# Kernel optimization log

Measured on AMD Instinct MI355X. Metric: run time of the kernel, lower is better.

The kernel has to match this reference:

```python
import jax, jax.numpy as jnp
import numpy as np

N_HEAD = 16
T0 = 1.0        # eta schedule reference time
C_LOG = 3.0     # fixed eta(t) = C_LOG * log(t / T0)  (mode='log', non-learnable default)
ETA_CLIP = 50.0 # eta clamped to [-ETA_CLIP, ETA_CLIP] before exponentiation


def setup_inputs() -> dict:
    key = jax.random.key(0)
    k0, k1, k2 = jax.random.split(key, 3)
    B, T, D = 2, 2048, 1024
    x = jax.random.normal(k0, (B, T, D), dtype=jnp.float32)
    ln_weight = jnp.ones((D,), dtype=jnp.float32)  # LayerNorm weight (bias=False per cfg)
    c_attn_w = jax.random.normal(k1, (3 * D, D), dtype=jnp.float32) * 0.02  # torch Linear weight [3D, D]
    c_proj_w = jax.random.normal(k2, (D, D), dtype=jnp.float32) * 0.02      # output proj [D, D]
    # theta_h = inv_softplus(1.0) so that step size h = softplus(theta_h) = 1.0
    theta_h = jnp.asarray(np.log(np.expm1(1.0)), dtype=jnp.float32)
    return {"x": x, "ln_weight": ln_weight, "c_attn_w": c_attn_w,
            "c_proj_w": c_proj_w, "theta_h": theta_h}


def _layer_norm(x, w, eps=1e-5):
    mu = jnp.mean(x, axis=-1, keepdims=True)
    var = jnp.var(x, axis=-1, keepdims=True)
    return (x - mu) * jax.lax.rsqrt(var + eps) * w


def reference(x, ln_weight, c_attn_w, c_proj_w, theta_h):
    B, T, D = x.shape
    H = N_HEAD
    hd = D // H

    y = _layer_norm(x, ln_weight)
    qkv = jnp.einsum('btd,ed->bte', y, c_attn_w)        # [B, T, 3D]
    q, k, v = jnp.split(qkv, 3, axis=-1)
    q = q.reshape(B, T, H, hd).transpose(0, 2, 1, 3)    # [B, H, T, hd]
    k = k.reshape(B, T, H, hd).transpose(0, 2, 1, 3)
    v = v.reshape(B, T, H, hd).transpose(0, 2, 1, 3)

    # time-dependent conformal/symplectic scaling: t_i = t0 + h*i, eta = c_log*log(t/t0)
    h = jax.nn.softplus(theta_h)
    t = T0 + h * jnp.arange(T, dtype=jnp.float32)
    eta = jnp.clip(C_LOG * jnp.log(t / T0), -ETA_CLIP, ETA_CLIP)  # [T]
    q = q * jnp.exp(eta)[None, None, :, None]    # query scaled by exp(+eta(t_i))
    k = k * jnp.exp(-eta)[None, None, :, None]   # key scaled by exp(-eta(t_j))

    att = jnp.einsum('bhqd,bhkd->bhqk', q, k) / jnp.sqrt(jnp.float32(hd))
    mask = jnp.tril(jnp.ones((T, T), dtype=bool))  # causal: keep j <= i
    att = jnp.where(mask[None, None], att, -jnp.inf)
    att = jax.nn.softmax(att, axis=-1)

    out = jnp.einsum('bhqk,bhkd->bhqd', att, v)
    out = out.transpose(0, 2, 1, 3).reshape(B, T, D)
    return jnp.einsum('btd,ed->bte', out, c_proj_w)
```

## Files before the change

kernel.cpp:

```cpp
#include <hip/hip_runtime.h>
#include <stdint.h>
#include <stddef.h>

typedef __attribute__((ext_vector_type(8))) short short8;
typedef __attribute__((ext_vector_type(4))) float float4v;

#define T_SEQ 2048
#define D_MODEL 1024
#define NH 16
#define HD 64

static __device__ __forceinline__ unsigned short f2bf(float f) {
  unsigned u = __builtin_bit_cast(unsigned, f);
  u += 0x7fffu + ((u >> 16) & 1u);
  return (unsigned short)(u >> 16);
}
static __device__ __forceinline__ float bf2f(unsigned short h) {
  unsigned u = ((unsigned)h) << 16;
  return __builtin_bit_cast(float, u);
}
static __device__ __forceinline__ float4v mfma16(short8 a, short8 b, float4v c) {
  return __builtin_amdgcn_mfma_f32_16x16x32_bf16(a, b, c, 0, 0, 0);
}
static __device__ __forceinline__ void split3(float f, unsigned short& h0,
                                              unsigned short& h1, unsigned short& h2) {
  h0 = f2bf(f);
  float r1 = f - bf2f(h0);
  h1 = f2bf(r1);
  float r2 = r1 - bf2f(h1);
  h2 = f2bf(r2);
}
static __device__ __forceinline__ void split2(float f, unsigned short& h0, unsigned short& h1) {
  h0 = f2bf(f);
  h1 = f2bf(f - bf2f(h0));
}

static __device__ __forceinline__ void stage16(const unsigned short* g, unsigned short* l) {
#if __has_builtin(__builtin_amdgcn_global_load_lds)
  __builtin_amdgcn_global_load_lds(
      (const __attribute__((address_space(1))) unsigned int*)g,
      (__attribute__((address_space(3))) unsigned int*)l, 16, 0, 0);
#else
  *(short8*)l = *(const short8*)g;
#endif
}

__global__ void eta_kernel(const float* theta, float* E, float* Einv) {
  int i = blockIdx.x * blockDim.x + threadIdx.x;
  if (i >= T_SEQ) return;
  float th = theta[0];
  float h = log1pf(expf(th));
  float t = 1.0f + h * (float)i;
  float eta = 3.0f * logf(t);
  eta = fminf(fmaxf(eta, -50.0f), 50.0f);
  E[i] = expf(eta);
  Einv[i] = expf(-eta);
}

__global__ __launch_bounds__(256) void ln_kernel(const float* x, const float* wgt,
                          unsigned short* y0, unsigned short* y1, unsigned short* y2) {
  int row = blockIdx.x;
  int tid = threadIdx.x;
  const float* xr = x + (size_t)row * D_MODEL;
  float v[4];
  float sum = 0.f, ssq = 0.f;
  for (int it = 0; it < 4; ++it) {
    float f = xr[tid + 256 * it];
    v[it] = f;
    sum += f; ssq += f * f;
  }
  for (int off = 32; off >= 1; off >>= 1) {
    sum += __shfl_xor(sum, off, 64);
    ssq += __shfl_xor(ssq, off, 64);
  }
  __shared__ float rs[4], rq[4];
  int w = tid >> 6;
  if ((tid & 63) == 0) { rs[w] = sum; rq[w] = ssq; }
  __syncthreads();
  sum = rs[0] + rs[1] + rs[2] + rs[3];
  ssq = rq[0] + rq[1] + rq[2] + rq[3];
  float mu = sum * (1.0f / D_MODEL);
  float var = ssq * (1.0f / D_MODEL) - mu * mu;
  float rstd = rsqrtf(var + 1e-5f);
  for (int it = 0; it < 4; ++it) {
    int d = tid + 256 * it;
    float y = (v[it] - mu) * rstd * wgt[d];
    unsigned short h0, h1, h2;
    split3(y, h0, h1, h2);
    size_t o = (size_t)row * D_MODEL + d;
    y0[o] = h0; y1[o] = h1; y2[o] = h2;
  }
}

__global__ __launch_bounds__(256) void conv_w3(const float* src, unsigned short* W0,
                                               unsigned short* W1, unsigned short* W2) {
  size_t base = ((size_t)blockIdx.x * 256 + threadIdx.x) * 8;
  int row = (int)(base >> 10);
  short8 a, b, c;
  for (int j = 0; j < 8; ++j) {
    unsigned short h0, h1, h2;
    split3(src[base + j], h0, h1, h2);
    a[j] = (short)h0; b[j] = (short)h1; c[j] = (short)h2;
  }
  *(short8*)(W0 + base) = a;
  *(short8*)(W1 + base) = b;
  if (row < 2048) *(short8*)(W2 + base) = c;
}

__global__ __launch_bounds__(256) void conv_pw(const float* src, unsigned short* P0,
                                               unsigned short* P1) {
  size_t base = ((size_t)blockIdx.x * 256 + threadIdx.x) * 8;
  short8 a, b;
  for (int j = 0; j < 8; ++j) {
    unsigned short h0, h1;
    split2(src[base + j], h0, h1);
    a[j] = (short)h0; b[j] = (short)h1;
  }
  *(short8*)(P0 + base) = a;
  *(short8*)(P1 + base) = b;
}

__global__ __launch_bounds__(256) void qkv_qk(
    const unsigned short* y0, const unsigned short* y1, const unsigned short* y2,
    const unsigned short* W0, const unsigned short* W1, const unsigned short* W2,
    const float* E, const float* Einv,
    float* Qf, unsigned short* K0, unsigned short* K1, unsigned short* K2) {
  __shared__ unsigned short SB[6 * 4096];
  int tid = threadIdx.x;
  int w = tid >> 6, lane = tid & 63, q4 = lane >> 4, ln = lane & 15;
  int wr = w >> 1, wc = w & 1;
  int n0g = blockIdx.x * 128;
  int m0 = blockIdx.y * 128;
  const unsigned short* Asrc[3] = {y0, y1, y2};
  const unsigned short* Bsrc[3] = {W0, W1, W2};

  float4v zero = {0.f, 0.f, 0.f, 0.f};
  float4v acc[4][4];
  for (int mt = 0; mt < 4; ++mt)
    for (int ct = 0; ct < 4; ++ct) acc[mt][ct] = zero;

  int srow = tid >> 2;
  int kpart = tid & 3;
  unsigned lds_off = (unsigned)tid * 16;

  for (int k0 = 0; k0 < D_MODEL; k0 += 32) {
    __syncthreads();
    for (int i = 0; i < 2; ++i) {
      size_t arow = (size_t)(m0 + srow + i * 64) * D_MODEL + k0 + kpart * 8;
      size_t brow = (size_t)(n0g + srow + i * 64) * D_MODEL + k0 + kpart * 8;
      for (int s = 0; s < 3; ++s) {
        stage16(Asrc[s] + arow, (unsigned short*)((char*)(SB + s * 4096) + lds_off + i * 4096));
        stage16(Bsrc[s] + brow, (unsigned short*)((char*)(SB + (3 + s) * 4096) + lds_off + i * 4096));
      }
    }
    __syncthreads();

    short8 af[4][3];
    for (int mt = 0; mt < 4; ++mt)
      for (int s = 0; s < 3; ++s)
        af[mt][s] = *(const short8*)(SB + s * 4096 + (wr * 64 + mt * 16 + ln) * 32 + q4 * 8);
    for (int ct = 0; ct < 4; ++ct) {
      int brow = (wc * 64 + ct * 16 + ln) * 32 + q4 * 8;
      short8 b0 = *(const short8*)(SB + 3 * 4096 + brow);
      short8 b1 = *(const short8*)(SB + 4 * 4096 + brow);
      short8 b2 = *(const short8*)(SB + 5 * 4096 + brow);
      for (int mt = 0; mt < 4; ++mt) {
        float4v a = acc[mt][ct];
        a = mfma16(af[mt][0], b0, a);
        a = mfma16(af[mt][1], b0, a);
        a = mfma16(af[mt][0], b1, a);
        a = mfma16(af[mt][1], b1, a);
        a = mfma16(af[mt][0], b2, a);
        a = mfma16(af[mt][2], b0, a);
        acc[mt][ct] = a;
      }
    }
  }

  int region = n0g >> 10;
  int bi = m0 >> 11;
  int m0g = m0 & 2047;
  __syncthreads();
  if (region == 0) {
    float* Ql = (float*)SB;
    for (int h = 0; h < 2; ++h) {
      if (wc == h) {
        for (int mt = 0; mt < 4; ++mt)
          for (int ct = 0; ct < 4; ++ct)
            for (int r = 0; r < 4; ++r) {
              int t_loc = wr * 64 + mt * 16 + q4 * 4 + r;
              int d = ct * 16 + ln;
              int t = m0g + t_loc;
              Ql[t_loc * 64 + d] = acc[mt][ct][r] * (E[t] * 0.1803368801f);
            }
      }
      __syncthreads();
      int h_glob = ((n0g + h * 64) & 1023) >> 6;
      float* dst = Qf + ((size_t)(bi * NH + h_glob) * T_SEQ + m0g) * HD;
      for (int it = 0; it < 8; ++it) {
        int idx = it * 256 + tid;
        *(float4v*)(dst + idx * 4) = *(const float4v*)(Ql + idx * 4);
      }
      __syncthreads();
    }
  } else {
    unsigned short* Kl = SB;
    for (int h = 0; h < 2; ++h) {
      if (wc == h) {
        for (int mt = 0; mt < 4; ++mt)
          for (int ct = 0; ct < 4; ++ct)
            for (int r = 0; r < 4; ++r) {
              int t_loc = wr * 64 + mt * 16 + q4 * 4 + r;
              int d = ct * 16 + ln;
              int t = m0g + t_loc;
              unsigned short h0, h1, h2;
              split3(acc[mt][ct][r] * Einv[t], h0, h1, h2);
              Kl[t_loc * 64 + d] = h0;
              Kl[8192 + t_loc * 64 + d] = h1;
              Kl[16384 + t_loc * 64 + d] = h2;
            }
      }
      __syncthreads();
      int h_glob = ((n0g + h * 64) & 1023) >> 6;
      size_t base = ((size_t)(bi * NH + h_glob) * T_SEQ + m0g) * HD;
      unsigned short* dsts[3] = {K0 + base, K1 + base, K2 + base};
      for (int s = 0; s < 3; ++s)
        for (int it = 0; it < 4; ++it) {
          int idx = it * 256 + tid;
          *(short8*)(dsts[s] + idx * 8) = *(const short8*)(Kl + s * 8192 + idx * 8);
        }
      __syncthreads();
    }
  }
}

__global__ __launch_bounds__(256) void qkv_v(
    const unsigned short* y0, const unsigned short* y1,
    const unsigned short* W0, const unsigned short* W1, unsigned short* VbT) {
  __shared__ unsigned short SB[4 * 4096];
  int tid = threadIdx.x;
  int w = tid >> 6, lane = tid & 63, q4 = lane >> 4, ln = lane & 15;
  int wr = w >> 1, wc = w & 1;
  int n0g = blockIdx.x * 128;
  int m0 = blockIdx.y * 128;
  const unsigned short* Asrc[2] = {y0, y1};
  const unsigned short* Bsrc[2] = {W0, W1};

  float4v zero = {0.f, 0.f, 0.f, 0.f};
  float4v acc[4][4];
  for (int mt = 0; mt < 4; ++mt)
    for (int ct = 0; ct < 4; ++ct) acc[mt][ct] = zero;

  int srow = tid >> 2, kpart = tid & 3;
  unsigned lds_off = (unsigned)tid * 16;

  for (int k0 = 0; k0 < D_MODEL; k0 += 32) {
    __syncthreads();
    for (int i = 0; i < 2; ++i) {
      size_t arow = (size_t)(m0 + srow + i * 64) * D_MODEL + k0 + kpart * 8;
      size_t brow = (size_t)(2048 + n0g + srow + i * 64) * D_MODEL + k0 + kpart * 8;
      for (int s = 0; s < 2; ++s) {
        stage16(Asrc[s] + arow, (unsigned short*)((char*)(SB + s * 4096) + lds_off + i * 4096));
        stage16(Bsrc[s] + brow, (unsigned short*)((char*)(SB + (2 + s) * 4096) + lds_off + i * 4096));
      }
    }
    __syncthreads();

    short8 af[4][2];
    for (int mt = 0; mt < 4; ++mt)
      for (int s = 0; s < 2; ++s)
        af[mt][s] = *(const short8*)(SB + s * 4096 + (wr * 64 + mt * 16 + ln) * 32 + q4 * 8);
    for (int ct = 0; ct < 4; ++ct) {
      int brow = (wc * 64 + ct * 16 + ln) * 32 + q4 * 8;
      short8 b0 = *(const short8*)(SB + 2 * 4096 + brow);
      short8 b1 = *(const short8*)(SB + 3 * 4096 + brow);
      for (int mt = 0; mt < 4; ++mt) {
        float4v a = acc[mt][ct];
        a = mfma16(af[mt][0], b0, a);
        a = mfma16(af[mt][1], b0, a);
        a = mfma16(af[mt][0], b1, a);
        acc[mt][ct] = a;
      }
    }
  }

  int bi = m0 >> 11;
  int m0g = m0 & 2047;
  __syncthreads();
  unsigned short* Vl = SB;
  for (int h = 0; h < 2; ++h) {
    if (wc == h) {
      for (int mt = 0; mt < 4; ++mt)
        for (int ct = 0; ct < 4; ++ct)
          for (int r = 0; r < 4; ++r) {
            int t_loc = wr * 64 + mt * 16 + q4 * 4 + r;
            int d = ct * 16 + ln;
            Vl[d * 128 + t_loc] = f2bf(acc[mt][ct][r]);
          }
    }
    __syncthreads();
    int h_glob = (n0g + h * 64) >> 6;
    size_t base = (size_t)(bi * NH + h_glob) * HD * T_SEQ + m0g;
    for (int it = 0; it < 4; ++it) {
      int idx = it * 256 + tid;
      int d = idx >> 4, c = idx & 15;
      *(short8*)(VbT + base + (size_t)d * T_SEQ + c * 8) =
          *(const short8*)(Vl + d * 128 + c * 8);
    }
    __syncthreads();
  }
}

__global__ __launch_bounds__(256) void attn_kernel(
    const float* Qf, const unsigned short* K0, const unsigned short* K1,
    const unsigned short* K2, const unsigned short* VbT,
    unsigned short* Ob0, unsigned short* Ob1) {
  __shared__ unsigned short Ks[2][3][4096];
  __shared__ unsigned short Vs[2][4096];
  __shared__ unsigned short Plds[4][16][72];
  int tid = threadIdx.x;
  int w = tid >> 6, lane = tid & 63, q4 = lane >> 4, ln = lane & 15;
  int px = blockIdx.x;
  int bh = blockIdx.y;
  const float* Qb = Qf + (size_t)bh * T_SEQ * HD;
  const unsigned short* Kb0 = K0 + (size_t)bh * T_SEQ * HD;
  const unsigned short* Kb1 = K1 + (size_t)bh * T_SEQ * HD;
  const unsigned short* Kb2 = K2 + (size_t)bh * T_SEQ * HD;
  const unsigned short* Vb = VbT + (size_t)bh * HD * T_SEQ;
  int b = bh >> 4, hh = bh & 15;
  float4v zero = {0.f, 0.f, 0.f, 0.f};
  short8 ones;
  for (int j = 0; j < 8; ++j) ones[j] = (short)(unsigned short)0x3F80;

  int srow = tid >> 3, scs = tid & 7;
  int scd = scs ^ (srow & 7);
  int swz = ln & 7;

  for (int half = 0; half < 2; ++half) {
    int qt = half ? (31 - px) : px;
    int q0 = qt * 64;
    int ibase = q0 + w * 16;

    short8 qa[2][3];
    {
      const float* qp = Qb + (size_t)(ibase + ln) * HD;
      for (int ks = 0; ks < 2; ++ks) {
        float f[8];
        *(float4v*)&f[0] = *(const float4v*)(qp + ks * 32 + q4 * 8);
        *(float4v*)&f[4] = *(const float4v*)(qp + ks * 32 + q4 * 8 + 4);
        for (int j = 0; j < 8; ++j) {
          unsigned short h0, h1, h2;
          split3(f[j], h0, h1, h2);
          qa[ks][0][j] = (short)h0; qa[ks][1][j] = (short)h1; qa[ks][2][j] = (short)h2;
        }
      }
    }

    float m_r[4] = {-3e38f, -3e38f, -3e38f, -3e38f};
    float4v lacc = zero;
    float4v oacc[4];
    for (int c = 0; c < 4; ++c) oacc[c] = zero;

    __syncthreads();
    for (int i = 0; i < 2; ++i) {
      size_t go = (size_t)(srow + i * 32) * 64 + scd * 8;
      int lo = tid * 8 + i * 2048;
      stage16(Kb0 + go, &Ks[0][0][lo]);
      stage16(Kb1 + go, &Ks[0][1][lo]);
      stage16(Kb2 + go, &Ks[0][2][lo]);
      stage16(Vb + (size_t)(srow + i * 32) * T_SEQ + scd * 8, &Vs[0][lo]);
    }

    for (int jt = 0; jt <= qt; ++jt) {
      int cur = jt & 1;
      int j0 = jt * 64;
      __syncthreads();
      if (jt < qt) {
        int jn = j0 + 64;
        for (int i = 0; i < 2; ++i) {
          size_t go = (size_t)(jn + srow + i * 32) * 64 + scd * 8;
          int lo = tid * 8 + i * 2048;
          stage16(Kb0 + go, &Ks[cur ^ 1][0][lo]);
          stage16(Kb1 + go, &Ks[cur ^ 1][1][lo]);
          stage16(Kb2 + go, &Ks[cur ^ 1][2][lo]);
          stage16(Vb + (size_t)(srow + i * 32) * T_SEQ + jn + scd * 8,
                  &Vs[cur ^ 1][lo]);
        }
      }
      bool diag = (jt == qt);
      float p[4][4];
      for (int c = 0; c < 4; ++c) {
        int jl = c * 16 + ln;
        float4v s = zero;
        for (int ks = 0; ks < 2; ++ks) {
          int koff = (jl * 8 + ((ks * 4 + q4) ^ swz)) * 8;
          short8 k0v = *(const short8*)&Ks[cur][0][koff];
          short8 k1v = *(const short8*)&Ks[cur][1][koff];
          short8 k2v = *(const short8*)&Ks[cur][2][koff];
          s = mfma16(qa[ks][0], k0v, s);
          s = mfma16(qa[ks][1], k0v, s);
          s = mfma16(qa[ks][0], k1v, s);
          s = mfma16(qa[ks][1], k1v, s);
          s = mfma16(qa[ks][0], k2v, s);
          s = mfma16(qa[ks][2], k0v, s);
        }
        int jrow = j0 + jl;
        for (int r = 0; r < 4; ++r) {
          float l = s[r];
          if (diag && jrow > ibase + q4 * 4 + r) l = -3e38f;
          p[c][r] = l;
        }
      }
      float alpha[4], mnew[4];
      for (int r = 0; r < 4; ++r) {
        float tm = fmaxf(fmaxf(p[0][r], p[1][r]), fmaxf(p[2][r], p[3][r]));
        for (int off = 8; off >= 1; off >>= 1) tm = fmaxf(tm, __shfl_xor(tm, off, 16));
        mnew[r] = fmaxf(m_r[r], tm);
        alpha[r] = exp2f(m_r[r] - mnew[r]);
        m_r[r] = mnew[r];
      }
      for (int c = 0; c < 4; ++c)
        for (int r = 0; r < 4; ++r)
          p[c][r] = exp2f(p[c][r] - mnew[r]);
      for (int c = 0; c < 4; ++c)
        for (int r = 0; r < 4; ++r) oacc[c][r] *= alpha[r];
      for (int r = 0; r < 4; ++r) lacc[r] *= alpha[r];

      __asm__ __volatile__("" ::: "memory");
      for (int c = 0; c < 4; ++c)
        for (int r = 0; r < 4; ++r)
          Plds[w][q4 * 4 + r][c * 16 + ln] = f2bf(p[c][r]);
      __asm__ __volatile__("" ::: "memory");

      for (int ks = 0; ks < 2; ++ks) {
        short8 pa = *(const short8*)&Plds[w][ln][ks * 32 + q4 * 8];
        for (int c = 0; c < 4; ++c) {
          int voff = ((c * 16 + ln) * 8 + ((ks * 4 + q4) ^ swz)) * 8;
          short8 vb = *(const short8*)&Vs[cur][voff];
          oacc[c] = mfma16(pa, vb, oacc[c]);
        }
        lacc = mfma16(pa, ones, lacc);
      }
      __asm__ __volatile__("" ::: "memory");
    }

    for (int c = 0; c < 4; ++c)
      for (int r = 0; r < 4; ++r) {
        int i = ibase + q4 * 4 + r;
        float val = oacc[c][r] / lacc[r];
        unsigned short h0, h1;
        split2(val, h0, h1);
        size_t o = ((size_t)(b * T_SEQ + i)) * D_MODEL + hh * 64 + c * 16 + ln;
        Ob0[o] = h0; Ob1[o] = h1;
      }
  }
}

__global__ __launch_bounds__(256) void proj_gemm(
    const unsigned short* A0, const unsigned short* A1,
    const unsigned short* P0, const unsigned short* P1, float* out) {
  __shared__ unsigned short SB[4 * 4096];
  int tid = threadIdx.x;
  int w = tid >> 6, lane = tid & 63, q4 = lane >> 4, ln = lane & 15;
  int wr = w >> 1, wc = w & 1;
  int n0g = blockIdx.x * 128;
  int m0 = blockIdx.y * 128;
  const unsigned short* Asrc[2] = {A0, A1};
  const unsigned short* Bsrc[2] = {P0, P1};

  float4v zero = {0.f, 0.f, 0.f, 0.f};
  float4v acc[4][4];
  for (int mt = 0; mt < 4; ++mt)
    for (int ct = 0; ct < 4; ++ct) acc[mt][ct] = zero;

  int srow = tid >> 2, kpart = tid & 3;
  unsigned lds_off = (unsigned)tid * 16;

  for (int k0 = 0; k0 < D_MODEL; k0 += 32) {
    __syncthreads();
    for (int i = 0; i < 2; ++i) {
      size_t arow = (size_t)(m0 + srow + i * 64) * D_MODEL + k0 + kpart * 8;
      size_t brow = (size_t)(n0g + srow + i * 64) * D_MODEL + k0 + kpart * 8;
      for (int s = 0; s < 2; ++s) {
        stage16(Asrc[s] + arow, (unsigned short*)((char*)(SB + s * 4096) + lds_off + i * 4096));
        stage16(Bsrc[s] + brow, (unsigned short*)((char*)(SB + (2 + s) * 4096) + lds_off + i * 4096));
      }
    }
    __syncthreads();

    short8 af[4][2];
    for (int mt = 0; mt < 4; ++mt)
      for (int s = 0; s < 2; ++s)
        af[mt][s] = *(const short8*)(SB + s * 4096 + (wr * 64 + mt * 16 + ln) * 32 + q4 * 8);
    for (int ct = 0; ct < 4; ++ct) {
      int brow = (wc * 64 + ct * 16 + ln) * 32 + q4 * 8;
      short8 b0 = *(const short8*)(SB + 2 * 4096 + brow);
      short8 b1 = *(const short8*)(SB + 3 * 4096 + brow);
      for (int mt = 0; mt < 4; ++mt) {
        float4v a = acc[mt][ct];
        a = mfma16(af[mt][0], b0, a);
        a = mfma16(af[mt][1], b0, a);
        a = mfma16(af[mt][0], b1, a);
        acc[mt][ct] = a;
      }
    }
  }

  for (int mt = 0; mt < 4; ++mt)
    for (int ct = 0; ct < 4; ++ct)
      for (int r = 0; r < 4; ++r) {
        int gm = m0 + wr * 64 + mt * 16 + q4 * 4 + r;
        int col = n0g + wc * 64 + ct * 16 + ln;
        out[(size_t)gm * D_MODEL + col] = acc[mt][ct][r];
      }
}

extern "C" void kernel_launch(void* const* d_in, const int* in_sizes, int n_in,
                              void* d_out, int out_size, void* d_ws, size_t ws_size,
                              hipStream_t stream) {
  const float* x      = (const float*)d_in[0];
  const float* ln_w   = (const float*)d_in[1];
  const float* attn_w = (const float*)d_in[2];
  const float* proj_w = (const float*)d_in[3];
  const float* theta  = (const float*)d_in[4];
  float* out = (float*)d_out;

  char* ws = (char*)d_ws;
  const size_t SZY  = (size_t)4096 * 1024 * 2;
  const size_t SZW  = (size_t)3072 * 1024 * 2;
  const size_t SZW2 = (size_t)2048 * 1024 * 2;
  const size_t SZQ  = (size_t)2 * 16 * 2048 * 64 * 4;
  const size_t SZK  = (size_t)2 * 16 * 2048 * 64 * 2;

  unsigned short* y0 = (unsigned short*)(ws);
  unsigned short* y1 = (unsigned short*)(ws + SZY);
  unsigned short* y2 = (unsigned short*)(ws + 2 * SZY);
  unsigned short* W0 = (unsigned short*)(ws + 3 * SZY);
  unsigned short* W1 = (unsigned short*)(ws + 3 * SZY + SZW);
  unsigned short* W2 = (unsigned short*)(ws + 3 * SZY + 2 * SZW);
  float* Qf          = (float*)(ws + 3 * SZY + 2 * SZW + SZW2);
  unsigned short* K0 = (unsigned short*)(ws + 3 * SZY + 2 * SZW + SZW2 + SZQ);
  unsigned short* K1 = (unsigned short*)(ws + 3 * SZY + 2 * SZW + SZW2 + SZQ + SZK);
  float* E           = (float*)(ws + 3 * SZY + 2 * SZW + SZW2 + SZQ + 2 * SZK);
  float* Einv        = E + T_SEQ;
  unsigned short* Ob0 = y0;
  unsigned short* Ob1 = y1;
  unsigned short* PW0 = y2;
  unsigned short* PW1 = y2 + (size_t)1024 * 1024;
  unsigned short* VbT = (unsigned short*)d_out;
  unsigned short* K2  = (unsigned short*)((char*)d_out + SZK);

  size_t needed = 3 * SZY + 2 * SZW + SZW2 + SZQ + 2 * SZK + 2 * T_SEQ * 4;
  if (ws_size < needed) return;

  eta_kernel<<<dim3(8), dim3(256), 0, stream>>>(theta, E, Einv);
  ln_kernel<<<dim3(4096), dim3(256), 0, stream>>>(x, ln_w, y0, y1, y2);
  conv_w3<<<dim3(1536), dim3(256), 0, stream>>>(attn_w, W0, W1, W2);
  qkv_qk<<<dim3(16, 32), dim3(256), 0, stream>>>(y0, y1, y2, W0, W1, W2, E, Einv,
                                                 Qf, K0, K1, K2);
  qkv_v<<<dim3(8, 32), dim3(256), 0, stream>>>(y0, y1, W0, W1, VbT);
  attn_kernel<<<dim3(16, 32), dim3(256), 0, stream>>>(Qf, K0, K1, K2, VbT, Ob0, Ob1);
  conv_pw<<<dim3(512), dim3(256), 0, stream>>>(proj_w, PW0, PW1);
  proj_gemm<<<dim3(8, 32), dim3(256), 0, stream>>>(Ob0, Ob1, PW0, PW1, out);
}
```

Baseline: 381.8 us.

## Merge prep kernels and QKV GEMMs, restructure attention loop with specialized diagonal step

Folds the eta, layernorm and weight-split kernels into one launch, and the QK and V projection GEMMs into a single grid, cutting launch count and tail gaps between kernels. In attention, the masked diagonal tile is peeled out of the loop so off-diagonal tiles skip the mask check. The P-to-bf16 conversion now truncates instead of rounding. The grid becomes 1D with a remapped head/tile order that interleaves heads across blocks. The truncation slightly changes numerics, and the combined GEMM grid mixes blocks of unequal cost.

```diff
diff --git a/kernel.cpp b/kernel.cpp
--- a/kernel.cpp
+++ b/kernel.cpp
@@ -45,66 +45,68 @@
 #endif
 }
 
-__global__ void eta_kernel(const float* theta, float* E, float* Einv) {
-  int i = blockIdx.x * blockDim.x + threadIdx.x;
-  if (i >= T_SEQ) return;
-  float th = theta[0];
-  float h = log1pf(expf(th));
-  float t = 1.0f + h * (float)i;
-  float eta = 3.0f * logf(t);
-  eta = fminf(fmaxf(eta, -50.0f), 50.0f);
-  E[i] = expf(eta);
-  Einv[i] = expf(-eta);
-}
-
-__global__ __launch_bounds__(256) void ln_kernel(const float* x, const float* wgt,
-                          unsigned short* y0, unsigned short* y1, unsigned short* y2) {
-  int row = blockIdx.x;
+__global__ __launch_bounds__(256) void prep_kernel(
+    const float* x, const float* wgt, const float* attn_w, const float* theta,
+    unsigned short* y0, unsigned short* y1, unsigned short* y2,
+    unsigned short* W0, unsigned short* W1, unsigned short* W2,
+    float* E, float* Einv) {
+  __shared__ float rs[4], rq[4];
+  int bx = blockIdx.x;
   int tid = threadIdx.x;
-  const float* xr = x + (size_t)row * D_MODEL;
-  float v[4];
-  float sum = 0.f, ssq = 0.f;
-  for (int it = 0; it < 4; ++it) {
-    float f = xr[tid + 256 * it];
-    v[it] = f;
-    sum += f; ssq += f * f;
-  }
-  for (int off = 32; off >= 1; off >>= 1) {
-    sum += __shfl_xor(sum, off, 64);
-    ssq += __shfl_xor(ssq, off, 64);
-  }
-  __shared__ float rs[4], rq[4];
-  int w = tid >> 6;
-  if ((tid & 63) == 0) { rs[w] = sum; rq[w] = ssq; }
-  __syncthreads();
-  sum = rs[0] + rs[1] + rs[2] + rs[3];
-  ssq = rq[0] + rq[1] + rq[2] + rq[3];
-  float mu = sum * (1.0f / D_MODEL);
-  float var = ssq * (1.0f / D_MODEL) - mu * mu;
-  float rstd = rsqrtf(var + 1e-5f);
-  for (int it = 0; it < 4; ++it) {
-    int d = tid + 256 * it;
-    float y = (v[it] - mu) * rstd * wgt[d];
-    unsigned short h0, h1, h2;
-    split3(y, h0, h1, h2);
-    size_t o = (size_t)row * D_MODEL + d;
-    y0[o] = h0; y1[o] = h1; y2[o] = h2;
-  }
-}
-
-__global__ __launch_bounds__(256) void conv_w3(const float* src, unsigned short* W0,
-                                               unsigned short* W1, unsigned short* W2) {
-  size_t base = ((size_t)blockIdx.x * 256 + threadIdx.x) * 8;
-  int row = (int)(base >> 10);
-  short8 a, b, c;
-  for (int j = 0; j < 8; ++j) {
-    unsigned short h0, h1, h2;
-    split3(src[base + j], h0, h1, h2);
-    a[j] = (short)h0; b[j] = (short)h1; c[j] = (short)h2;
-  }
-  *(short8*)(W0 + base) = a;
-  *(short8*)(W1 + base) = b;
-  if (row < 2048) *(short8*)(W2 + base) = c;
+  if (bx < 4096) {
+    int row = bx;
+    const float* xr = x + (size_t)row * D_MODEL;
+    float v[4];
+    float sum = 0.f, ssq = 0.f;
+    for (int it = 0; it < 4; ++it) {
+      float f = xr[tid + 256 * it];
+      v[it] = f;
+      sum += f; ssq += f * f;
+    }
+    for (int off = 32; off >= 1; off >>= 1) {
+      sum += __shfl_xor(sum, off, 64);
+      ssq += __shfl_xor(ssq, off, 64);
+    }
+    int w = tid >> 6;
+    if ((tid & 63) == 0) { rs[w] = sum; rq[w] = ssq; }
+    __syncthreads();
+    sum = rs[0] + rs[1] + rs[2] + rs[3];
+    ssq = rq[0] + rq[1] + rq[2] + rq[3];
+    float mu = sum * (1.0f / D_MODEL);
+    float var = ssq * (1.0f / D_MODEL) - mu * mu;
+    float rstd = rsqrtf(var + 1e-5f);
+    for (int it = 0; it < 4; ++it) {
+      int d = tid + 256 * it;
+      float y = (v[it] - mu) * rstd * wgt[d];
+      unsigned short h0, h1, h2;
+      split3(y, h0, h1, h2);
+      size_t o = (size_t)row * D_MODEL + d;
+      y0[o] = h0; y1[o] = h1; y2[o] = h2;
+    }
+  } else if (bx < 5632) {
+    size_t base = ((size_t)(bx - 4096) * 256 + tid) * 8;
+    int row = (int)(base >> 10);
+    short8 a, b, c;
+    for (int j = 0; j < 8; ++j) {
+      unsigned short h0, h1, h2;
+      split3(attn_w[base + j], h0, h1, h2);
+      a[j] = (short)h0; b[j] = (short)h1; c[j] = (short)h2;
+    }
+    *(short8*)(W0 + base) = a;
+    *(short8*)(W1 + base) = b;
+    if (row < 2048) *(short8*)(W2 + base) = c;
+  } else {
+    int i = (bx - 5632) * 256 + tid;
+    if (i < T_SEQ) {
+      float th = theta[0];
+      float h = log1pf(expf(th));
+      float t = 1.0f + h * (float)i;
+      float eta = 3.0f * logf(t);
+      eta = fminf(fmaxf(eta, -50.0f), 50.0f);
+      E[i] = expf(eta);
+      Einv[i] = expf(-eta);
+    }
+  }
 }
 
 __global__ __launch_bounds__(256) void conv_pw(const float* src, unsigned short* P0,
@@ -120,69 +122,149 @@
   *(short8*)(P1 + base) = b;
 }
 
-__global__ __launch_bounds__(256) void qkv_qk(
+__global__ __launch_bounds__(256) void qkv_gemm(
     const unsigned short* y0, const unsigned short* y1, const unsigned short* y2,
     const unsigned short* W0, const unsigned short* W1, const unsigned short* W2,
     const float* E, const float* Einv,
-    float* Qf, unsigned short* K0, unsigned short* K1, unsigned short* K2) {
+    float* Qf, unsigned short* K0, unsigned short* K1, unsigned short* K2,
+    unsigned short* VbT) {
   __shared__ unsigned short SB[6 * 4096];
   int tid = threadIdx.x;
   int w = tid >> 6, lane = tid & 63, q4 = lane >> 4, ln = lane & 15;
   int wr = w >> 1, wc = w & 1;
-  int n0g = blockIdx.x * 128;
   int m0 = blockIdx.y * 128;
-  const unsigned short* Asrc[3] = {y0, y1, y2};
-  const unsigned short* Bsrc[3] = {W0, W1, W2};
-
+  int bi = m0 >> 11;
+  int m0g = m0 & 2047;
+  int srow = tid >> 2, kpart = tid & 3;
+  unsigned lds_off = (unsigned)tid * 16;
   float4v zero = {0.f, 0.f, 0.f, 0.f};
   float4v acc[4][4];
   for (int mt = 0; mt < 4; ++mt)
     for (int ct = 0; ct < 4; ++ct) acc[mt][ct] = zero;
 
-  int srow = tid >> 2;
-  int kpart = tid & 3;
-  unsigned lds_off = (unsigned)tid * 16;
-
-  for (int k0 = 0; k0 < D_MODEL; k0 += 32) {
-    __syncthreads();
-    for (int i = 0; i < 2; ++i) {
-      size_t arow = (size_t)(m0 + srow + i * 64) * D_MODEL + k0 + kpart * 8;
-      size_t brow = (size_t)(n0g + srow + i * 64) * D_MODEL + k0 + kpart * 8;
-      for (int s = 0; s < 3; ++s) {
-        stage16(Asrc[s] + arow, (unsigned short*)((char*)(SB + s * 4096) + lds_off + i * 4096));
-        stage16(Bsrc[s] + brow, (unsigned short*)((char*)(SB + (3 + s) * 4096) + lds_off + i * 4096));
-      }
-    }
-    __syncthreads();
-
-    short8 af[4][3];
-    for (int mt = 0; mt < 4; ++mt)
-      for (int s = 0; s < 3; ++s)
-        af[mt][s] = *(const short8*)(SB + s * 4096 + (wr * 64 + mt * 16 + ln) * 32 + q4 * 8);
-    for (int ct = 0; ct < 4; ++ct) {
-      int brow = (wc * 64 + ct * 16 + ln) * 32 + q4 * 8;
-      short8 b0 = *(const short8*)(SB + 3 * 4096 + brow);
-      short8 b1 = *(const short8*)(SB + 4 * 4096 + brow);
-      short8 b2 = *(const short8*)(SB + 5 * 4096 + brow);
-      for (int mt = 0; mt < 4; ++mt) {
-        float4v a = acc[mt][ct];
-        a = mfma16(af[mt][0], b0, a);
-        a = mfma16(af[mt][1], b0, a);
-        a = mfma16(af[mt][0], b1, a);
-        a = mfma16(af[mt][1], b1, a);
-        a = mfma16(af[mt][0], b2, a);
-        a = mfma16(af[mt][2], b0, a);
-        acc[mt][ct] = a;
-      }
-    }
-  }
-
-  int region = n0g >> 10;
-  int bi = m0 >> 11;
-  int m0g = m0 & 2047;
-  __syncthreads();
-  if (region == 0) {
-    float* Ql = (float*)SB;
+  if (blockIdx.x < 16) {
+    int n0g = blockIdx.x * 128;
+    const unsigned short* Asrc[3] = {y0, y1, y2};
+    const unsigned short* Bsrc[3] = {W0, W1, W2};
+    for (int k0 = 0; k0 < D_MODEL; k0 += 32) {
+      __syncthreads();
+      for (int i = 0; i < 2; ++i) {
+        size_t arow = (size_t)(m0 + srow + i * 64) * D_MODEL + k0 + kpart * 8;
+        size_t brow = (size_t)(n0g + srow + i * 64) * D_MODEL + k0 + kpart * 8;
+        for (int s = 0; s < 3; ++s) {
+          stage16(Asrc[s] + arow, (unsigned short*)((char*)(SB + s * 4096) + lds_off + i * 4096));
+          stage16(Bsrc[s] + brow, (unsigned short*)((char*)(SB + (3 + s) * 4096) + lds_off + i * 4096));
+        }
+      }
+      __syncthreads();
+      short8 af[4][3];
+      for (int mt = 0; mt < 4; ++mt)
+        for (int s = 0; s < 3; ++s)
+          af[mt][s] = *(const short8*)(SB + s * 4096 + (wr * 64 + mt * 16 + ln) * 32 + q4 * 8);
+      for (int ct = 0; ct < 4; ++ct) {
+        int brow = (wc * 64 + ct * 16 + ln) * 32 + q4 * 8;
+        short8 b0 = *(const short8*)(SB + 3 * 4096 + brow);
+        short8 b1 = *(const short8*)(SB + 4 * 4096 + brow);
+        short8 b2 = *(const short8*)(SB + 5 * 4096 + brow);
+        for (int mt = 0; mt < 4; ++mt) {
+          float4v a = acc[mt][ct];
+          a = mfma16(af[mt][0], b0, a);
+          a = mfma16(af[mt][1], b0, a);
+          a = mfma16(af[mt][0], b1, a);
+          a = mfma16(af[mt][1], b1, a);
+          a = mfma16(af[mt][0], b2, a);
+          a = mfma16(af[mt][2], b0, a);
+          acc[mt][ct] = a;
+        }
+      }
+    }
+    int region = n0g >> 10;
+    __syncthreads();
+    if (region == 0) {
+      float* Ql = (float*)SB;
+      for (int h = 0; h < 2; ++h) {
+        if (wc == h) {
+          for (int mt = 0; mt < 4; ++mt)
+            for (int ct = 0; ct < 4; ++ct)
+              for (int r = 0; r < 4; ++r) {
+                int t_loc = wr * 64 + mt * 16 + q4 * 4 + r;
+                int d = ct * 16 + ln;
+                int t = m0g + t_loc;
+                Ql[t_loc * 64 + d] = acc[mt][ct][r] * (E[t] * 0.1803368801f);
+              }
+        }
+        __syncthreads();
+        int h_glob = ((n0g + h * 64) & 1023) >> 6;
+        float* dst = Qf + ((size_t)(bi * NH + h_glob) * T_SEQ + m0g) * HD;
+        for (int it = 0; it < 8; ++it) {
+          int idx = it * 256 + tid;
+          *(float4v*)(dst + idx * 4) = *(const float4v*)(Ql + idx * 4);
+        }
+        __syncthreads();
+      }
+    } else {
+      unsigned short* Kl = SB;
+      for (int h = 0; h < 2; ++h) {
+        if (wc == h) {
+          for (int mt = 0; mt < 4; ++mt)
+            for (int ct = 0; ct < 4; ++ct)
+              for (int r = 0; r < 4; ++r) {
+                int t_loc = wr * 64 + mt * 16 + q4 * 4 + r;
+                int d = ct * 16 + ln;
+                int t = m0g + t_loc;
+                unsigned short h0, h1, h2;
+                split3(acc[mt][ct][r] * Einv[t], h0, h1, h2);
+                Kl[t_loc * 64 + d] = h0;
+                Kl[8192 + t_loc * 64 + d] = h1;
+                Kl[16384 + t_loc * 64 + d] = h2;
+              }
+        }
+        __syncthreads();
+        int h_glob = ((n0g + h * 64) & 1023) >> 6;
+        size_t base = ((size_t)(bi * NH + h_glob) * T_SEQ + m0g) * HD;
+        unsigned short* dsts[3] = {K0 + base, K1 + base, K2 + base};
+        for (int s = 0; s < 3; ++s)
+          for (int it = 0; it < 4; ++it) {
+            int idx = it * 256 + tid;
+            *(short8*)(dsts[s] + idx * 8) = *(const short8*)(Kl + s * 8192 + idx * 8);
+          }
+        __syncthreads();
+      }
+    }
+  } else {
+    int n0g = (blockIdx.x - 16) * 128;
+    const unsigned short* Asrc[2] = {y0, y1};
+    const unsigned short* Bsrc[2] = {W0, W1};
+    for (int k0 = 0; k0 < D_MODEL; k0 += 32) {
+      __syncthreads();
+      for (int i = 0; i < 2; ++i) {
+        size_t arow = (size_t)(m0 + srow + i * 64) * D_MODEL + k0 + kpart * 8;
+        size_t brow = (size_t)(2048 + n0g + srow + i * 64) * D_MODEL + k0 + kpart * 8;
+        for (int s = 0; s < 2; ++s) {
+          stage16(Asrc[s] + arow, (unsigned short*)((char*)(SB + s * 4096) + lds_off + i * 4096));
+          stage16(Bsrc[s] + brow, (unsigned short*)((char*)(SB + (2 + s) * 4096) + lds_off + i * 4096));
+        }
+      }
+      __syncthreads();
+      short8 af[4][2];
+      for (int mt = 0; mt < 4; ++mt)
+        for (int s = 0; s < 2; ++s)
+          af[mt][s] = *(const short8*)(SB + s * 4096 + (wr * 64 + mt * 16 + ln) * 32 + q4 * 8);
+      for (int ct = 0; ct < 4; ++ct) {
+        int brow = (wc * 64 + ct * 16 + ln) * 32 + q4 * 8;
+        short8 b0 = *(const short8*)(SB + 2 * 4096 + brow);
+        short8 b1 = *(const short8*)(SB + 3 * 4096 + brow);
+        for (int mt = 0; mt < 4; ++mt) {
+          float4v a = acc[mt][ct];
+          a = mfma16(af[mt][0], b0, a);
+          a = mfma16(af[mt][1], b0, a);
+          a = mfma16(af[mt][0], b1, a);
+          acc[mt][ct] = a;
+        }
+      }
+    }
+    __syncthreads();
+    unsigned short* Vl = SB;
     for (int h = 0; h < 2; ++h) {
       if (wc == h) {
         for (int mt = 0; mt < 4; ++mt)
@@ -190,126 +272,90 @@
             for (int r = 0; r < 4; ++r) {
               int t_loc = wr * 64 + mt * 16 + q4 * 4 + r;
               int d = ct * 16 + ln;
-              int t = m0g + t_loc;
-              Ql[t_loc * 64 + d] = acc[mt][ct][r] * (E[t] * 0.1803368801f);
+              Vl[d * 128 + t_loc] = f2bf(acc[mt][ct][r]);
             }
       }
       __syncthreads();
-      int h_glob = ((n0g + h * 64) & 1023) >> 6;
-      float* dst = Qf + ((size_t)(bi * NH + h_glob) * T_SEQ + m0g) * HD;
-      for (int it = 0; it < 8; ++it) {
+      int h_glob = (n0g + h * 64) >> 6;
+      size_t base = (size_t)(bi * NH + h_glob) * HD * T_SEQ + m0g;
+      for (int it = 0; it < 4; ++it) {
         int idx = it * 256 + tid;
-        *(float4v*)(dst + idx * 4) = *(const float4v*)(Ql + idx * 4);
-      }
-      __syncthreads();
-    }
-  } else {
-    unsigned short* Kl = SB;
-    for (int h = 0; h < 2; ++h) {
-      if (wc == h) {
-        for (int mt = 0; mt < 4; ++mt)
-          for (int ct = 0; ct < 4; ++ct)
-            for (int r = 0; r < 4; ++r) {
-              int t_loc = wr * 64 + mt * 16 + q4 * 4 + r;
-              int d = ct * 16 + ln;
-              int t = m0g + t_loc;
-              unsigned short h0, h1, h2;
-              split3(acc[mt][ct][r] * Einv[t], h0, h1, h2);
-              Kl[t_loc * 64 + d] = h0;
-              Kl[8192 + t_loc * 64 + d] = h1;
-              Kl[16384 + t_loc * 64 + d] = h2;
-            }
-      }
-      __syncthreads();
-      int h_glob = ((n0g + h * 64) & 1023) >> 6;
-      size_t base = ((size_t)(bi * NH + h_glob) * T_SEQ + m0g) * HD;
-      unsigned short* dsts[3] = {K0 + base, K1 + base, K2 + base};
-      for (int s = 0; s < 3; ++s)
-        for (int it = 0; it < 4; ++it) {
-          int idx = it * 256 + tid;
-          *(short8*)(dsts[s] + idx * 8) = *(const short8*)(Kl + s * 8192 + idx * 8);
-        }
-      __syncthreads();
-    }
-  }
-}
-
-__global__ __launch_bounds__(256) void qkv_v(
-    const unsigned short* y0, const unsigned short* y1,
-    const unsigned short* W0, const unsigned short* W1, unsigned short* VbT) {
-  __shared__ unsigned short SB[4 * 4096];
-  int tid = threadIdx.x;
-  int w = tid >> 6, lane = tid & 63, q4 = lane >> 4, ln = lane & 15;
-  int wr = w >> 1, wc = w & 1;
-  int n0g = blockIdx.x * 128;
-  int m0 = blockIdx.y * 128;
-  const unsigned short* Asrc[2] = {y0, y1};
-  const unsigned short* Bsrc[2] = {W0, W1};
-
-  float4v zero = {0.f, 0.f, 0.f, 0.f};
-  float4v acc[4][4];
-  for (int mt = 0; mt < 4; ++mt)
-    for (int ct = 0; ct < 4; ++ct) acc[mt][ct] = zero;
-
-  int srow = tid >> 2, kpart = tid & 3;
-  unsigned lds_off = (unsigned)tid * 16;
-
-  for (int k0 = 0; k0 < D_MODEL; k0 += 32) {
-    __syncthreads();
-    for (int i = 0; i < 2; ++i) {
-      size_t arow = (size_t)(m0 + srow + i * 64) * D_MODEL + k0 + kpart * 8;
-      size_t brow = (size_t)(2048 + n0g + srow + i * 64) * D_MODEL + k0 + kpart * 8;
-      for (int s = 0; s < 2; ++s) {
-        stage16(Asrc[s] + arow, (unsigned short*)((char*)(SB + s * 4096) + lds_off + i * 4096));
-        stage16(Bsrc[s] + brow, (unsigned short*)((char*)(SB + (2 + s) * 4096) + lds_off + i * 4096));
-      }
-    }
-    __syncthreads();
-
-    short8 af[4][2];
-    for (int mt = 0; mt < 4; ++mt)
-      for (int s = 0; s < 2; ++s)
-        af[mt][s] = *(const short8*)(SB + s * 4096 + (wr * 64 + mt * 16 + ln) * 32 + q4 * 8);
-    for (int ct = 0; ct < 4; ++ct) {
-      int brow = (wc * 64 + ct * 16 + ln) * 32 + q4 * 8;
-      short8 b0 = *(const short8*)(SB + 2 * 4096 + brow);
-      short8 b1 = *(const short8*)(SB + 3 * 4096 + brow);
-      for (int mt = 0; mt < 4; ++mt) {
-        float4v a = acc[mt][ct];
-        a = mfma16(af[mt][0], b0, a);
-        a = mfma16(af[mt][1], b0, a);
-        a = mfma16(af[mt][0], b1, a);
-        acc[mt][ct] = a;
-      }
-    }
-  }
-
-  int bi = m0 >> 11;
-  int m0g = m0 & 2047;
-  __syncthreads();
-  unsigned short* Vl = SB;
-  for (int h = 0; h < 2; ++h) {
-    if (wc == h) {
-      for (int mt = 0; mt < 4; ++mt)
-        for (int ct = 0; ct < 4; ++ct)
-          for (int r = 0; r < 4; ++r) {
-            int t_loc = wr * 64 + mt * 16 + q4 * 4 + r;
-            int d = ct * 16 + ln;
-            Vl[d * 128 + t_loc] = f2bf(acc[mt][ct][r]);
-          }
-    }
-    __syncthreads();
-    int h_glob = (n0g + h * 64) >> 6;
-    size_t base = (size_t)(bi * NH + h_glob) * HD * T_SEQ + m0g;
-    for (int it = 0; it < 4; ++it) {
-      int idx = it * 256 + tid;
-      int d = idx >> 4, c = idx & 15;
-      *(short8*)(VbT + base + (size_t)d * T_SEQ + c * 8) =
-          *(const short8*)(Vl + d * 128 + c * 8);
-    }
-    __syncthreads();
-  }
-}
+        int d = idx >> 4, c = idx & 15;
+        *(short8*)(VbT + base + (size_t)d * T_SEQ + c * 8) =
+            *(const short8*)(Vl + d * 128 + c * 8);
+      }
+      __syncthreads();
+    }
+  }
+}
+
+#define ATTN_STAGE(BUF, J0)                                                   \
+  for (int i_ = 0; i_ < 2; ++i_) {                                            \
+    size_t go_ = (size_t)((J0) + srow + i_ * 32) * 64 + scd * 8;              \
+    int lo_ = tid * 8 + i_ * 2048;                                            \
+    stage16(Kb0 + go_, &Ks[BUF][0][lo_]);                                     \
+    stage16(Kb1 + go_, &Ks[BUF][1][lo_]);                                     \
+    stage16(Kb2 + go_, &Ks[BUF][2][lo_]);                                     \
+    stage16(Vb + (size_t)(srow + i_ * 32) * T_SEQ + (J0) + scd * 8,           \
+            &Vs[BUF][lo_]);                                                   \
+  }
+
+#define ATTN_STEP(JT, DIAG)                                                   \
+  {                                                                           \
+    const int cur_ = (JT) & 1;                                                \
+    float p[4][4];                                                            \
+    for (int c = 0; c < 4; ++c) {                                             \
+      float4v s = zero;                                                       \
+      for (int ks = 0; ks < 2; ++ks) {                                        \
+        int koff = ((c * 16 + ln) * 8 + ((ks * 4 + q4) ^ swz)) * 8;           \
+        short8 k0v = *(const short8*)&Ks[cur_][0][koff];                      \
+        short8 k1v = *(const short8*)&Ks[cur_][1][koff];                      \
+        short8 k2v = *(const short8*)&Ks[cur_][2][koff];                      \
+        s = mfma16(qa[ks][0], k0v, s);                                        \
+        s = mfma16(qa[ks][1], k0v, s);                                        \
+        s = mfma16(qa[ks][0], k1v, s);                                        \
+        s = mfma16(qa[ks][1], k1v, s);                                        \
+        s = mfma16(qa[ks][0], k2v, s);                                        \
+        s = mfma16(qa[ks][2], k0v, s);                                        \
+      }                                                                       \
+      if (DIAG) {                                                             \
+        int jrow = (JT) * 64 + c * 16 + ln;                                   \
+        for (int r = 0; r < 4; ++r)                                           \
+          if (jrow > ibase + q4 * 4 + r) s[r] = -3e38f;                       \
+      }                                                                       \
+      for (int r = 0; r < 4; ++r) p[c][r] = s[r];                             \
+    }                                                                         \
+    float alpha[4], mnew[4];                                                  \
+    for (int r = 0; r < 4; ++r) {                                             \
+      float tm = fmaxf(fmaxf(p[0][r], p[1][r]), fmaxf(p[2][r], p[3][r]));     \
+      for (int off = 8; off >= 1; off >>= 1)                                  \
+        tm = fmaxf(tm, __shfl_xor(tm, off, 16));                              \
+      mnew[r] = fmaxf(m_r[r], tm);                                            \
+      alpha[r] = exp2f(m_r[r] - mnew[r]);                                     \
+      m_r[r] = mnew[r];                                                       \
+    }                                                                         \
+    for (int c = 0; c < 4; ++c)                                               \
+      for (int r = 0; r < 4; ++r) p[c][r] = exp2f(p[c][r] - mnew[r]);         \
+    for (int c = 0; c < 4; ++c)                                               \
+      for (int r = 0; r < 4; ++r) oacc[c][r] *= alpha[r];                     \
+    for (int r = 0; r < 4; ++r) lacc[r] *= alpha[r];                          \
+    __asm__ __volatile__("" ::: "memory");                                    \
+    for (int c = 0; c < 4; ++c)                                               \
+      for (int r = 0; r < 4; ++r)                                             \
+        Plds[w][q4 * 4 + r][c * 16 + ln] =                                    \
+            (unsigned short)(__builtin_bit_cast(unsigned, p[c][r]) >> 16);    \
+    __asm__ __volatile__("" ::: "memory");                                    \
+    for (int ks = 0; ks < 2; ++ks) {                                          \
+      short8 pa = *(const short8*)&Plds[w][ln][ks * 32 + q4 * 8];             \
+      for (int c = 0; c < 4; ++c) {                                           \
+        int voff = ((c * 16 + ln) * 8 + ((ks * 4 + q4) ^ swz)) * 8;           \
+        short8 vb = *(const short8*)&Vs[cur_][voff];                          \
+        oacc[c] = mfma16(pa, vb, oacc[c]);                                    \
+      }                                                                       \
+      lacc = mfma16(pa, ones, lacc);                                          \
+    }                                                                         \
+    __asm__ __volatile__("" ::: "memory");                                    \
+  }
 
 __global__ __launch_bounds__(256) void attn_kernel(
     const float* Qf, const unsigned short* K0, const unsigned short* K1,
@@ -320,8 +366,9 @@
   __shared__ unsigned short Plds[4][16][72];
   int tid = threadIdx.x;
   int w = tid >> 6, lane = tid & 63, q4 = lane >> 4, ln = lane & 15;
-  int px = blockIdx.x;
-  int bh = blockIdx.y;
+  int bidx = blockIdx.x;
+  int bh = ((bidx & 7) << 2) | ((bidx >> 3) & 3);
+  int px = bidx >> 5;
   const float* Qb = Qf + (size_t)bh * T_SEQ * HD;
   const unsigned short* Kb0 = K0 + (size_t)bh * T_SEQ * HD;
   const unsigned short* Kb1 = K1 + (size_t)bh * T_SEQ * HD;
@@ -362,87 +409,14 @@
     for (int c = 0; c < 4; ++c) oacc[c] = zero;
 
     __syncthreads();
-    for (int i = 0; i < 2; ++i) {
-      size_t go = (size_t)(srow + i * 32) * 64 + scd * 8;
-      int lo = tid * 8 + i * 2048;
-      stage16(Kb0 + go, &Ks[0][0][lo]);
-      stage16(Kb1 + go, &Ks[0][1][lo]);
-      stage16(Kb2 + go, &Ks[0][2][lo]);
-      stage16(Vb + (size_t)(srow + i * 32) * T_SEQ + scd * 8, &Vs[0][lo]);
-    }
-
-    for (int jt = 0; jt <= qt; ++jt) {
-      int cur = jt & 1;
-      int j0 = jt * 64;
-      __syncthreads();
-      if (jt < qt) {
-        int jn = j0 + 64;
-        for (int i = 0; i < 2; ++i) {
-          size_t go = (size_t)(jn + srow + i * 32) * 64 + scd * 8;
-          int lo = tid * 8 + i * 2048;
-          stage16(Kb0 + go, &Ks[cur ^ 1][0][lo]);
-          stage16(Kb1 + go, &Ks[cur ^ 1][1][lo]);
-          stage16(Kb2 + go, &Ks[cur ^ 1][2][lo]);
-          stage16(Vb + (size_t)(srow + i * 32) * T_SEQ + jn + scd * 8,
-                  &Vs[cur ^ 1][lo]);
-        }
-      }
-      bool diag = (jt == qt);
-      float p[4][4];
-      for (int c = 0; c < 4; ++c) {
-        int jl = c * 16 + ln;
-        float4v s = zero;
-        for (int ks = 0; ks < 2; ++ks) {
-          int koff = (jl * 8 + ((ks * 4 + q4) ^ swz)) * 8;
-          short8 k0v = *(const short8*)&Ks[cur][0][koff];
-          short8 k1v = *(const short8*)&Ks[cur][1][koff];
-          short8 k2v = *(const short8*)&Ks[cur][2][koff];
-          s = mfma16(qa[ks][0], k0v, s);
-          s = mfma16(qa[ks][1], k0v, s);
-          s = mfma16(qa[ks][0], k1v, s);
-          s = mfma16(qa[ks][1], k1v, s);
-          s = mfma16(qa[ks][0], k2v, s);
-          s = mfma16(qa[ks][2], k0v, s);
-        }
-        int jrow = j0 + jl;
-        for (int r = 0; r < 4; ++r) {
-          float l = s[r];
-          if (diag && jrow > ibase + q4 * 4 + r) l = -3e38f;
-          p[c][r] = l;
-        }
-      }
-      float alpha[4], mnew[4];
-      for (int r = 0; r < 4; ++r) {
-        float tm = fmaxf(fmaxf(p[0][r], p[1][r]), fmaxf(p[2][r], p[3][r]));
-        for (int off = 8; off >= 1; off >>= 1) tm = fmaxf(tm, __shfl_xor(tm, off, 16));
-        mnew[r] = fmaxf(m_r[r], tm);
-        alpha[r] = exp2f(m_r[r] - mnew[r]);
-        m_r[r] = mnew[r];
-      }
-      for (int c = 0; c < 4; ++c)
-        for (int r = 0; r < 4; ++r)
-          p[c][r] = exp2f(p[c][r] - mnew[r]);
-      for (int c = 0; c < 4; ++c)
-        for (int r = 0; r < 4; ++r) oacc[c][r] *= alpha[r];
-      for (int r = 0; r < 4; ++r) lacc[r] *= alpha[r];
-
-      __asm__ __volatile__("" ::: "memory");
-      for (int c = 0; c < 4; ++c)
-        for (int r = 0; r < 4; ++r)
-          Plds[w][q4 * 4 + r][c * 16 + ln] = f2bf(p[c][r]);
-      __asm__ __volatile__("" ::: "memory");
-
-      for (int ks = 0; ks < 2; ++ks) {
-        short8 pa = *(const short8*)&Plds[w][ln][ks * 32 + q4 * 8];
-        for (int c = 0; c < 4; ++c) {
-          int voff = ((c * 16 + ln) * 8 + ((ks * 4 + q4) ^ swz)) * 8;
-          short8 vb = *(const short8*)&Vs[cur][voff];
-          oacc[c] = mfma16(pa, vb, oacc[c]);
-        }
-        lacc = mfma16(pa, ones, lacc);
-      }
-      __asm__ __volatile__("" ::: "memory");
-    }
+    ATTN_STAGE(0, 0)
+    for (int jt = 0; jt < qt; ++jt) {
+      __syncthreads();
+      ATTN_STAGE((jt + 1) & 1, (jt + 1) * 64)
+      ATTN_STEP(jt, 0)
+    }
+    __syncthreads();
+    ATTN_STEP(qt, 1)
 
     for (int c = 0; c < 4; ++c)
       for (int r = 0; r < 4; ++r) {
@@ -455,6 +429,8 @@
       }
   }
 }
+#undef ATTN_STAGE
+#undef ATTN_STEP
 
 __global__ __launch_bounds__(256) void proj_gemm(
     const unsigned short* A0, const unsigned short* A1,
@@ -553,13 +529,11 @@
   size_t needed = 3 * SZY + 2 * SZW + SZW2 + SZQ + 2 * SZK + 2 * T_SEQ * 4;
   if (ws_size < needed) return;
 
-  eta_kernel<<<dim3(8), dim3(256), 0, stream>>>(theta, E, Einv);
-  ln_kernel<<<dim3(4096), dim3(256), 0, stream>>>(x, ln_w, y0, y1, y2);
-  conv_w3<<<dim3(1536), dim3(256), 0, stream>>>(attn_w, W0, W1, W2);
-  qkv_qk<<<dim3(16, 32), dim3(256), 0, stream>>>(y0, y1, y2, W0, W1, W2, E, Einv,
-                                                 Qf, K0, K1, K2);
-  qkv_v<<<dim3(8, 32), dim3(256), 0, stream>>>(y0, y1, W0, W1, VbT);
-  attn_kernel<<<dim3(16, 32), dim3(256), 0, stream>>>(Qf, K0, K1, K2, VbT, Ob0, Ob1);
+  prep_kernel<<<dim3(5640), dim3(256), 0, stream>>>(x, ln_w, attn_w, theta,
+                                                    y0, y1, y2, W0, W1, W2, E, Einv);
+  qkv_gemm<<<dim3(24, 32), dim3(256), 0, stream>>>(y0, y1, y2, W0, W1, W2, E, Einv,
+                                                   Qf, K0, K1, K2, VbT);
   conv_pw<<<dim3(512), dim3(256), 0, stream>>>(proj_w, PW0, PW1);
+  attn_kernel<<<dim3(512), dim3(256), 0, stream>>>(Qf, K0, K1, K2, VbT, Ob0, Ob1);
   proj_gemm<<<dim3(8, 32), dim3(256), 0, stream>>>(Ob0, Ob1, PW0, PW1, out);
 }
```

New measurement: 375.3 us. Within noise of the previous version (-1.7%).
